# Optimization experiments

Hardware: AMD Instinct MI355X
Metric: run time of the kernel (lower is better)

The kernel has to match this reference:

```python
import jax, jax.numpy as jnp
import numpy as np

# ---- static ragged feature layout (from CTGAN metadata) ----
NUM_CLUSTERS = [10, 8, 10, 5, 10, 10, 7, 10, 10, 10]          # per numerical feature
NUM_CATEGORIES = [2, 5, 10, 3, 50, 4, 2, 8, 100, 6, 2, 3, 12, 5, 2, 30, 4, 9, 2, 7]
TAU = 0.2        # GumbelSoftmax temperature (teras default)
BN_EPS = 1e-3    # keras BatchNormalization default epsilon
LATENT_DIM = 128
BATCH = 65536

_seg, _alpha = [], []
_gid = 0
for c in NUM_CLUSTERS:
    _seg.append(_gid); _alpha.append(True); _gid += 1        # alpha scalar (tanh), own segment
    _seg += [_gid] * c; _alpha += [False] * c; _gid += 1     # beta cluster group (gumbel softmax)
for k in NUM_CATEGORIES:
    _seg += [_gid] * k; _alpha += [False] * k; _gid += 1     # categorical group (gumbel softmax)
SEG = jnp.asarray(np.array(_seg, dtype=np.int32))
ALPHA_MASK = jnp.asarray(np.array(_alpha, dtype=bool))
N_SEG = _gid
DATA_DIM = len(_seg)  # 366


def setup_inputs() -> dict:
    key = jax.random.key(0)
    ks = jax.random.split(key, 8)
    z = jax.random.normal(ks[0], (BATCH, LATENT_DIM), dtype=jnp.float32)
    # pre-sampled standard Gumbel noise for the gumbel-softmax groups
    u = jax.random.uniform(ks[1], (BATCH, DATA_DIM), dtype=jnp.float32, minval=1e-6, maxval=1.0 - 1e-6)
    g = -jnp.log(-jnp.log(u))
    def w(k, fi, fo):
        return jax.random.normal(k, (fi, fo), dtype=jnp.float32) * (1.0 / np.sqrt(fi))
    return {
        "z": z, "g": g,
        "W1": w(ks[2], LATENT_DIM, 256), "b1": jnp.zeros((256,), jnp.float32),
        "gamma1": jnp.ones((256,), jnp.float32), "beta1": jnp.zeros((256,), jnp.float32),
        "W2": w(ks[3], LATENT_DIM + 256, 256), "b2": jnp.zeros((256,), jnp.float32),
        "gamma2": jnp.ones((256,), jnp.float32), "beta2": jnp.zeros((256,), jnp.float32),
        "Wout": w(ks[4], LATENT_DIM + 512, DATA_DIM), "bout": jnp.zeros((DATA_DIM,), jnp.float32),
    }


def _bn_relu(h, gamma, beta):
    # training-mode batch norm (batch statistics), as used while training CTGAN
    mu = jnp.mean(h, axis=0)
    var = jnp.var(h, axis=0)
    return jax.nn.relu((h - mu) * jax.lax.rsqrt(var + BN_EPS) * gamma + beta)


def reference(z, g, W1, b1, gamma1, beta1, W2, b2, gamma2, beta2, Wout, bout):
    # CTGAN residual generator layers: out = concat([relu(bn(dense(x))), x])
    h1 = jnp.concatenate([_bn_relu(z @ W1 + b1, gamma1, beta1), z], axis=1)    # [B, 384]
    h2 = jnp.concatenate([_bn_relu(h1 @ W2 + b2, gamma2, beta2), h1], axis=1)  # [B, 640]
    logits = h2 @ Wout + bout                                                  # [B, 366]

    # ragged per-group gumbel-softmax: segment-wise stable softmax over columns
    zt = ((logits + g) / TAU).T                                   # [D, B]
    m = jax.ops.segment_max(zt, SEG, num_segments=N_SEG)          # [S, B]
    e = jnp.exp(zt - m[SEG])
    s = jax.ops.segment_sum(e, SEG, num_segments=N_SEG)
    soft = (e / s[SEG]).T                                         # [B, D]
    # alpha columns: tanh of raw logits; all other columns: group softmax
    return jnp.where(ALPHA_MASK[None, :], jnp.tanh(logits), soft)
```

## Files before the change

kernel.cpp:

```cpp
#include <hip/hip_runtime.h>

typedef _Float16 half_t;
typedef _Float16 half4 __attribute__((ext_vector_type(4)));
typedef _Float16 half8 __attribute__((ext_vector_type(8)));
typedef float f32x4 __attribute__((ext_vector_type(4)));

#define AS1 __attribute__((address_space(1)))
#define AS3 __attribute__((address_space(3)))

static constexpr int NBATCH = 65536;

__global__ __launch_bounds__(256) void k_cvtz(const float* __restrict__ z,
                                              half_t* __restrict__ dst) {
  size_t i = (size_t)blockIdx.x * 256 + threadIdx.x;
  int row = (int)(i >> 4), c8 = (int)(i & 15) << 3;
  const float* s = z + (size_t)row * 128 + c8;
  float4 v0 = *(const float4*)s;
  float4 v1 = *(const float4*)(s + 4);
  half8 h;
  h[0]=(half_t)v0.x; h[1]=(half_t)v0.y; h[2]=(half_t)v0.z; h[3]=(half_t)v0.w;
  h[4]=(half_t)v1.x; h[5]=(half_t)v1.y; h[6]=(half_t)v1.z; h[7]=(half_t)v1.w;
  *(half8*)(dst + (size_t)row * 640 + c8) = h;
}

__global__ __launch_bounds__(256) void k_transpose(const float* __restrict__ W,
                                                   half_t* __restrict__ Wt,
                                                   int K, int N, int total) {
  int i = blockIdx.x * 256 + threadIdx.x;
  if (i >= total) return;
  int n = i / K;
  int k = i - n * K;
  float v = (n < N) ? W[k * N + n] : 0.f;
  Wt[i] = (half_t)v;
}

template<bool STATS, bool F16OUT>
__global__ __launch_bounds__(256) void k_gemm(
    const half_t* __restrict__ A, int lda, int K,
    const half_t* __restrict__ Bt,
    const float* __restrict__ bias,
    half_t* __restrict__ o16, float* __restrict__ o32, int ldo, int ncreal,
    float* __restrict__ ps, float* __restrict__ pq) {
  __shared__ __align__(16) char smem[32768];
  const int tid  = threadIdx.x;
  const int lane = tid & 63;
  const int w    = tid >> 6;
  const int wr   = w >> 1, wc = w & 1;
  const int ml   = lane & 15, g = lane >> 4;
  const int brow = blockIdx.x * 128;
  const int bcol = blockIdx.y * 128;
  const int sr  = lane >> 3;
  const int scg = (lane & 7) ^ sr;

  f32x4 acc[4][4];
#pragma unroll
  for (int i = 0; i < 4; i++)
#pragma unroll
    for (int j = 0; j < 4; j++) acc[i][j] = (f32x4){0.f, 0.f, 0.f, 0.f};

  const half_t* Abase = A  + (size_t)brow * lda;
  const half_t* Bbase = Bt + (size_t)bcol * K;
  const int nt = K >> 6;

  half_t* As = (half_t*)smem;
  half_t* Bs = (half_t*)(smem + 16384);

  for (int t = 0; t < nt; t++) {
    const int k0 = t * 64;
    if (t) __syncthreads();
#pragma unroll
    for (int it = 0; it < 4; it++) {
      int q = it * 4 + w;
      int r = q * 8 + sr;
      __builtin_amdgcn_global_load_lds(
          (AS1 const void*)(Abase + (size_t)r * lda + k0 + scg * 8),
          (AS3 void*)(As + q * 512), 16, 0, 0);
      __builtin_amdgcn_global_load_lds(
          (AS1 const void*)(Bbase + (size_t)r * K + k0 + scg * 8),
          (AS3 void*)(Bs + q * 512), 16, 0, 0);
    }
    __syncthreads();
#pragma unroll
    for (int t2 = 0; t2 < 2; t2++) {
      const int c4 = t2 * 4 + g;
      half8 af[4], bf[4];
#pragma unroll
      for (int fm = 0; fm < 4; fm++) {
        int row = wr * 64 + fm * 16 + ml;
        af[fm] = *(const half8*)((const char*)As + row * 128 + ((c4 ^ (row & 7)) << 4));
      }
#pragma unroll
      for (int fn = 0; fn < 4; fn++) {
        int row = wc * 64 + fn * 16 + ml;
        bf[fn] = *(const half8*)((const char*)Bs + row * 128 + ((c4 ^ (row & 7)) << 4));
      }
#pragma unroll
      for (int fm = 0; fm < 4; fm++)
#pragma unroll
        for (int fn = 0; fn < 4; fn++)
          acc[fm][fn] = __builtin_amdgcn_mfma_f32_16x16x32_f16(af[fm], bf[fn], acc[fm][fn], 0, 0, 0);
    }
  }
  __syncthreads();

#pragma unroll
  for (int fn = 0; fn < 4; fn++) {
    int col  = wc * 64 + fn * 16 + ml;
    int gcol = bcol + col;
    float bz = (gcol < ncreal) ? bias[gcol] : 0.f;
    float s = 0.f, q = 0.f;
#pragma unroll
    for (int fm = 0; fm < 4; fm++)
#pragma unroll
      for (int rr = 0; rr < 4; rr++) {
        float v = acc[fm][fn][rr] + bz;
        acc[fm][fn][rr] = v;
        if (STATS) { s += v; q += v * v; }
      }
    if (STATS) {
      s += __shfl_xor(s, 16, 64); s += __shfl_xor(s, 32, 64);
      q += __shfl_xor(q, 16, 64); q += __shfl_xor(q, 32, 64);
      if (g == 0) {
        ps[(size_t)gcol * 1024 + blockIdx.x * 2 + wr] = s;
        pq[(size_t)gcol * 1024 + blockIdx.x * 2 + wr] = q;
      }
    }
  }

  if (F16OUT) {
    half_t* so = (half_t*)smem;
#pragma unroll
    for (int fn = 0; fn < 4; fn++)
#pragma unroll
      for (int fm = 0; fm < 4; fm++)
#pragma unroll
        for (int rr = 0; rr < 4; rr++)
          so[(wr * 64 + fm * 16 + g * 4 + rr) * 128 + wc * 64 + fn * 16 + ml] =
              (half_t)acc[fm][fn][rr];
    __syncthreads();
#pragma unroll
    for (int it = 0; it < 8; it++) {
      int r = it * 16 + (tid >> 4);
      int c = (tid & 15) * 8;
      *(half8*)(o16 + (size_t)(brow + r) * ldo + bcol + c) = *(const half8*)&so[r * 128 + c];
    }
  } else {
    float* so = (float*)smem;
    for (int h = 0; h < 2; h++) {
      if (wr == h) {
#pragma unroll
        for (int fn = 0; fn < 4; fn++)
#pragma unroll
          for (int fm = 0; fm < 4; fm++)
#pragma unroll
            for (int rr = 0; rr < 4; rr++)
              so[(fm * 16 + g * 4 + rr) * 128 + wc * 64 + fn * 16 + ml] = acc[fm][fn][rr];
      }
      __syncthreads();
      int r0 = h * 64;
      for (int i = tid; i < 64 * 64; i += 256) {
        int r  = i >> 6;
        int c2 = (i & 63) * 2;
        int gc = bcol + c2;
        if (gc < ncreal)
          *(float2*)(o32 + (size_t)(brow + r0 + r) * ldo + gc) = *(const float2*)&so[r * 128 + c2];
      }
      __syncthreads();
    }
  }
}

__global__ __launch_bounds__(256) void k_bnfinal(
    const float* __restrict__ ps, const float* __restrict__ pq,
    const float* __restrict__ gamma, const float* __restrict__ beta,
    float* __restrict__ sc, float* __restrict__ sh) {
  int c = blockIdx.x, t = threadIdx.x;
  float s = 0.f, q = 0.f;
#pragma unroll
  for (int i = 0; i < 4; i++) {
    s += ps[(size_t)c * 1024 + t + i * 256];
    q += pq[(size_t)c * 1024 + t + i * 256];
  }
#pragma unroll
  for (int o = 1; o < 64; o <<= 1) { s += __shfl_xor(s, o, 64); q += __shfl_xor(q, o, 64); }
  __shared__ float ss[4], qq[4];
  if ((t & 63) == 0) { ss[t >> 6] = s; qq[t >> 6] = q; }
  __syncthreads();
  if (t == 0) {
    s = ss[0] + ss[1] + ss[2] + ss[3];
    q = qq[0] + qq[1] + qq[2] + qq[3];
    float mu   = s * (1.f / NBATCH);
    float var  = fmaxf(q * (1.f / NBATCH) - mu * mu, 0.f);
    float rstd = rsqrtf(var + 1e-3f);
    float a = gamma[c] * rstd;
    sc[c] = a;
    sh[c] = beta[c] - mu * a;
  }
}

__global__ __launch_bounds__(256) void k_bnrelu(half_t* __restrict__ p,
                                                const float* __restrict__ sc,
                                                const float* __restrict__ sh) {
  size_t i = (size_t)blockIdx.x * 256 + threadIdx.x;
  int row = (int)(i >> 5), c8 = (int)(i & 31) << 3;
  half_t* a = p + (size_t)row * 640 + c8;
  half8 v = *(const half8*)a;
  half8 o;
#pragma unroll
  for (int j = 0; j < 8; j++)
    o[j] = (half_t)fmaxf(fmaf((float)v[j], sc[c8 + j], sh[c8 + j]), 0.f);
  *(half8*)a = o;
}

template<int L>
__device__ __forceinline__ void seg_rt(float* __restrict__ zr, int S) {
  float v[L];
#pragma unroll
  for (int j = 0; j < L; j++) v[j] = zr[S + j];
  float m0 = -1e30f, m1 = -1e30f, m2 = -1e30f, m3 = -1e30f;
#pragma unroll
  for (int j = 0; j < L; j++) {
    if ((j & 3) == 0) m0 = fmaxf(m0, v[j]);
    else if ((j & 3) == 1) m1 = fmaxf(m1, v[j]);
    else if ((j & 3) == 2) m2 = fmaxf(m2, v[j]);
    else m3 = fmaxf(m3, v[j]);
  }
  const float m = fmaxf(fmaxf(m0, m1), fmaxf(m2, m3));
  float s0 = 0.f, s1 = 0.f, s2 = 0.f, s3 = 0.f;
#pragma unroll
  for (int j = 0; j < L; j++) {
    float e = __expf(v[j] - m);
    v[j] = e;
    if ((j & 3) == 0) s0 += e;
    else if ((j & 3) == 1) s1 += e;
    else if ((j & 3) == 2) s2 += e;
    else s3 += e;
  }
  const float inv = 1.0f / ((s0 + s1) + (s2 + s3));
#pragma unroll
  for (int j = 0; j < L; j++) zr[S + j] = v[j] * inv;
}

template<int L>
__device__ __forceinline__ void seg_pad(float* __restrict__ zr, int S, int Lr) {
  float v[L];
#pragma unroll
  for (int j = 0; j < L; j++) v[j] = (j < Lr) ? zr[S + j] : -1e30f;
  float m = -1e30f;
#pragma unroll
  for (int j = 0; j < L; j++) m = fmaxf(m, v[j]);
  float s = 0.f;
#pragma unroll
  for (int j = 0; j < L; j++) {
    float e = __expf(v[j] - m);
    v[j] = e;
    s += e;
  }
  const float inv = 1.0f / s;
#pragma unroll
  for (int j = 0; j < L; j++)
    if (j < Lr) zr[S + j] = v[j] * inv;
}

template<int S, int L>
__device__ __forceinline__ void seg_split(float* __restrict__ zr, int par) {
  constexpr int H = L / 2;
  const int base = S + par * H;
  float v[H];
#pragma unroll
  for (int j = 0; j < H; j++) v[j] = zr[base + j];
  float m = -1e30f;
#pragma unroll
  for (int j = 0; j < H; j++) m = fmaxf(m, v[j]);
  m = fmaxf(m, __shfl_xor(m, 1, 64));
  float s = 0.f;
#pragma unroll
  for (int j = 0; j < H; j++) {
    float e = __expf(v[j] - m);
    v[j] = e;
    s += e;
  }
  s += __shfl_xor(s, 1, 64);
  const float inv = 1.0f / s;
#pragma unroll
  for (int j = 0; j < H; j++) zr[base + j] = v[j] * inv;
}

template<int H>
__device__ __forceinline__ void seg_quad(float* __restrict__ zr, int base, int n) {
  float v[H];
#pragma unroll
  for (int j = 0; j < H; j++) v[j] = (j < n) ? zr[base + j] : -1e30f;
  float m = -1e30f;
#pragma unroll
  for (int j = 0; j < H; j++) m = fmaxf(m, v[j]);
  m = fmaxf(m, __shfl_xor(m, 1, 64));
  m = fmaxf(m, __shfl_xor(m, 2, 64));
  float s = 0.f;
#pragma unroll
  for (int j = 0; j < H; j++) {
    float e = __expf(v[j] - m);
    v[j] = e;
    s += e;
  }
  s += __shfl_xor(s, 1, 64);
  s += __shfl_xor(s, 2, 64);
  const float inv = 1.0f / s;
#pragma unroll
  for (int j = 0; j < H; j++)
    if (j < n) zr[base + j] = v[j] * inv;
}

__device__ __forceinline__ bool is_alpha(int c) {
  const unsigned long long AM0 =
      (1ull << 0) | (1ull << 11) | (1ull << 20) | (1ull << 31) | (1ull << 37) |
      (1ull << 48) | (1ull << 59);
  const unsigned long long AM1 = (1ull << 3) | (1ull << 14) | (1ull << 25);
  if (c >= 90) return false;
  return (((c < 64) ? (AM0 >> c) : (AM1 >> (c - 64))) & 1ull) != 0ull;
}

__global__ __launch_bounds__(512, 2) void k_softmax(const float* __restrict__ g,
                                                    float* __restrict__ out) {
  __shared__ float zb[32][373];
  const int tid = threadIdx.x;
  const size_t gbase = (size_t)blockIdx.x * 32 * 366;
  for (int i2 = tid; i2 < 32 * 183; i2 += 512) {
    int e0 = i2 * 2;
    int r = e0 / 366;
    int c = e0 - r * 366;
    float2 lg = *(const float2*)(out + gbase + e0);
    float2 gg = *(const float2*)(g + gbase + e0);
    zb[r][c]     = is_alpha(c)     ? tanhf(lg.x) : (lg.x + gg.x) * 5.0f;
    zb[r][c + 1] = is_alpha(c + 1) ? tanhf(lg.y) : (lg.y + gg.y) * 5.0f;
  }
  __syncthreads();
  {
    const int lane = tid & 63;
    const int w    = tid >> 6;
    const int par  = lane & 1;
    if (w < 4) {
      const int quad = lane & 3;
      float* zr = &zb[(w & 1) * 16 + (lane >> 2)][0];
      if (w < 2) {
        seg_quad<25>(zr, 184 + quad * 25, 25);
      } else {
        seg_quad<13>(zr, 120 + quad * 13 - (quad >> 1) * (quad & 1), 13 - (quad >> 1));
        seg_rt<10>(zr, par ? 68 : 1);
      }
    } else {
      float* zr = &zb[lane >> 1][0];
      switch (w) {
        case 4: seg_split<314, 30>(zr, par);
                seg_rt<7>(zr, par ? 359 : 60);
                seg_rt<2>(zr, par ? 174 : 100);
                seg_rt<2>(zr, par ? 312 : 290); break;
        case 5: seg_rt<10>(zr, par ? 90 : 38);
                seg_rt<10>(zr, par ? 107 : 49);
                seg_pad<2>(zr, par ? 357 : 0, par ? 2 : 0); break;
        case 6: seg_pad<12>(zr, par ? 348 : 295, par ? 9 : 12);
                seg_pad<6>(zr, par ? 284 : 32, par ? 6 : 5);
                seg_rt<5>(zr, par ? 307 : 102); break;
        default: seg_rt<10>(zr, par ? 79 : 21);
                 seg_rt<8>(zr, par ? 176 : 12);
                 seg_rt<4>(zr, par ? 344 : 170);
                 seg_rt<3>(zr, par ? 292 : 117); break;
      }
    }
  }
  __syncthreads();
  for (int i2 = tid; i2 < 32 * 183; i2 += 512) {
    int e0 = i2 * 2;
    int r = e0 / 366;
    int c = e0 - r * 366;
    float2 o;
    o.x = zb[r][c];
    o.y = zb[r][c + 1];
    *(float2*)(out + gbase + e0) = o;
  }
}

extern "C" void kernel_launch(void* const* d_in, const int* in_sizes, int n_in,
                              void* d_out, int out_size, void* d_ws, size_t ws_size,
                              hipStream_t stream) {
  const float* z      = (const float*)d_in[0];
  const float* g      = (const float*)d_in[1];
  const float* W1     = (const float*)d_in[2];
  const float* b1     = (const float*)d_in[3];
  const float* gamma1 = (const float*)d_in[4];
  const float* beta1  = (const float*)d_in[5];
  const float* W2     = (const float*)d_in[6];
  const float* b2     = (const float*)d_in[7];
  const float* gamma2 = (const float*)d_in[8];
  const float* beta2  = (const float*)d_in[9];
  const float* Wout   = (const float*)d_in[10];
  const float* bout   = (const float*)d_in[11];
  float* out = (float*)d_out;
  char* ws = (char*)d_ws;

  size_t off = 0;
  half_t* act = (half_t*)(ws + off); off += (size_t)NBATCH * 640 * 2;
  half_t* W1t = (half_t*)(ws + off); off += (size_t)256 * 128 * 2;
  half_t* W2t = (half_t*)(ws + off); off += (size_t)256 * 384 * 2;
  half_t* Wot = (half_t*)(ws + off); off += (size_t)384 * 640 * 2;
  float*  ps  = (float*)(ws + off);  off += (size_t)256 * 1024 * 4;
  float*  pq  = (float*)(ws + off);  off += (size_t)256 * 1024 * 4;
  float*  sc1 = (float*)(ws + off);  off += 256 * 4;
  float*  sh1 = (float*)(ws + off);  off += 256 * 4;
  float*  sc2 = (float*)(ws + off);  off += 256 * 4;
  float*  sh2 = (float*)(ws + off);  off += 256 * 4;
  (void)ws_size; (void)in_sizes; (void)n_in; (void)out_size;

  k_cvtz<<<4096, 256, 0, stream>>>(z, act + 512);
  k_transpose<<<(256 * 128 + 255) / 256, 256, 0, stream>>>(W1, W1t, 128, 256, 256 * 128);
  k_transpose<<<(256 * 384 + 255) / 256, 256, 0, stream>>>(W2, W2t, 384, 256, 256 * 384);
  k_transpose<<<(384 * 640 + 255) / 256, 256, 0, stream>>>(Wout, Wot, 640, 366, 384 * 640);

  k_gemm<true, true><<<dim3(512, 2), 256, 0, stream>>>(
      act + 512, 640, 128, W1t, b1, act + 256, nullptr, 640, 256, ps, pq);
  k_bnfinal<<<256, 256, 0, stream>>>(ps, pq, gamma1, beta1, sc1, sh1);
  k_bnrelu<<<8192, 256, 0, stream>>>(act + 256, sc1, sh1);

  k_gemm<true, true><<<dim3(512, 2), 256, 0, stream>>>(
      act + 256, 640, 384, W2t, b2, act + 0, nullptr, 640, 256, ps, pq);
  k_bnfinal<<<256, 256, 0, stream>>>(ps, pq, gamma2, beta2, sc2, sh2);
  k_bnrelu<<<8192, 256, 0, stream>>>(act + 0, sc2, sh2);

  k_gemm<false, false><<<dim3(512, 3), 256, 0, stream>>>(
      act, 640, 640, Wot, bout, nullptr, out, 366, 366, nullptr, nullptr);

  k_softmax<<<NBATCH / 32, 512, 0, stream>>>(g, out);
}
```

Baseline: 199.4 us.

## Move tanh into GEMM epilogue and run segment softmax directly on global memory

The tanh for alpha columns moves into the output GEMM epilogue. The softmax kernel drops its shared-memory staging and instead reads logits and Gumbel noise straight from global memory per segment, writing results back in place. Occupancy hints rise from 2 to 6 blocks per SM. This removes the LDS round trip and two barriers. In exchange, global accesses become strided per-row, scalar and uncoalesced, which may hurt memory efficiency.

Measured after the change: 279.2 us. +40.0%, slower.

```diff
diff --git a/kernel.cpp b/kernel.cpp
--- a/kernel.cpp
+++ b/kernel.cpp
@@ -9,6 +9,15 @@
 #define AS3 __attribute__((address_space(3)))
 
 static constexpr int NBATCH = 65536;
+
+__device__ __forceinline__ bool is_alpha(int c) {
+  const unsigned long long AM0 =
+      (1ull << 0) | (1ull << 11) | (1ull << 20) | (1ull << 31) | (1ull << 37) |
+      (1ull << 48) | (1ull << 59);
+  const unsigned long long AM1 = (1ull << 3) | (1ull << 14) | (1ull << 25);
+  if (c >= 90) return false;
+  return (((c < 64) ? (AM0 >> c) : (AM1 >> (c - 64))) & 1ull) != 0ull;
+}
 
 __global__ __launch_bounds__(256) void k_cvtz(const float* __restrict__ z,
                                               half_t* __restrict__ dst) {
@@ -162,8 +171,14 @@
         int r  = i >> 6;
         int c2 = (i & 63) * 2;
         int gc = bcol + c2;
-        if (gc < ncreal)
-          *(float2*)(o32 + (size_t)(brow + r0 + r) * ldo + gc) = *(const float2*)&so[r * 128 + c2];
+        if (gc < ncreal) {
+          float2 v = *(const float2*)&so[r * 128 + c2];
+          if (gc < 90) {
+            if (is_alpha(gc))     v.x = tanhf(v.x);
+            if (is_alpha(gc + 1)) v.y = tanhf(v.y);
+          }
+          *(float2*)(o32 + (size_t)(brow + r0 + r) * ldo + gc) = v;
+        }
       }
       __syncthreads();
     }
@@ -213,84 +228,71 @@
 }
 
 template<int L>
-__device__ __forceinline__ void seg_rt(float* __restrict__ zr, int S) {
+__device__ __forceinline__ void gseg_rt(float* __restrict__ zo,
+                                        const float* __restrict__ zg, int S) {
   float v[L];
 #pragma unroll
-  for (int j = 0; j < L; j++) v[j] = zr[S + j];
-  float m0 = -1e30f, m1 = -1e30f, m2 = -1e30f, m3 = -1e30f;
-#pragma unroll
-  for (int j = 0; j < L; j++) {
-    if ((j & 3) == 0) m0 = fmaxf(m0, v[j]);
-    else if ((j & 3) == 1) m1 = fmaxf(m1, v[j]);
-    else if ((j & 3) == 2) m2 = fmaxf(m2, v[j]);
-    else m3 = fmaxf(m3, v[j]);
-  }
-  const float m = fmaxf(fmaxf(m0, m1), fmaxf(m2, m3));
-  float s0 = 0.f, s1 = 0.f, s2 = 0.f, s3 = 0.f;
-#pragma unroll
-  for (int j = 0; j < L; j++) {
-    float e = __expf(v[j] - m);
-    v[j] = e;
-    if ((j & 3) == 0) s0 += e;
-    else if ((j & 3) == 1) s1 += e;
-    else if ((j & 3) == 2) s2 += e;
-    else s3 += e;
-  }
-  const float inv = 1.0f / ((s0 + s1) + (s2 + s3));
-#pragma unroll
-  for (int j = 0; j < L; j++) zr[S + j] = v[j] * inv;
-}
-
-template<int L>
-__device__ __forceinline__ void seg_pad(float* __restrict__ zr, int S, int Lr) {
-  float v[L];
-#pragma unroll
-  for (int j = 0; j < L; j++) v[j] = (j < Lr) ? zr[S + j] : -1e30f;
+  for (int j = 0; j < L; j++) v[j] = (zo[S + j] + zg[S + j]) * 5.0f;
   float m = -1e30f;
 #pragma unroll
   for (int j = 0; j < L; j++) m = fmaxf(m, v[j]);
   float s = 0.f;
 #pragma unroll
-  for (int j = 0; j < L; j++) {
-    float e = __expf(v[j] - m);
-    v[j] = e;
-    s += e;
-  }
+  for (int j = 0; j < L; j++) { float e = __expf(v[j] - m); v[j] = e; s += e; }
   const float inv = 1.0f / s;
 #pragma unroll
+  for (int j = 0; j < L; j++) zo[S + j] = v[j] * inv;
+}
+
+template<int L>
+__device__ __forceinline__ void gseg_pad(float* __restrict__ zo,
+                                         const float* __restrict__ zg,
+                                         int S, int Lr) {
+  float v[L];
+#pragma unroll
   for (int j = 0; j < L; j++)
-    if (j < Lr) zr[S + j] = v[j] * inv;
+    v[j] = (j < Lr) ? (zo[S + j] + zg[S + j]) * 5.0f : -1e30f;
+  float m = -1e30f;
+#pragma unroll
+  for (int j = 0; j < L; j++) m = fmaxf(m, v[j]);
+  float s = 0.f;
+#pragma unroll
+  for (int j = 0; j < L; j++) { float e = __expf(v[j] - m); v[j] = e; s += e; }
+  const float inv = 1.0f / s;
+#pragma unroll
+  for (int j = 0; j < L; j++)
+    if (j < Lr) zo[S + j] = v[j] * inv;
 }
 
 template<int S, int L>
-__device__ __forceinline__ void seg_split(float* __restrict__ zr, int par) {
+__device__ __forceinline__ void gseg_split(float* __restrict__ zo,
+                                           const float* __restrict__ zg, int par) {
   constexpr int H = L / 2;
-  const int base = S + par * H;
+  const int b = S + par * H;
   float v[H];
 #pragma unroll
-  for (int j = 0; j < H; j++) v[j] = zr[base + j];
+  for (int j = 0; j < H; j++) v[j] = (zo[b + j] + zg[b + j]) * 5.0f;
   float m = -1e30f;
 #pragma unroll
   for (int j = 0; j < H; j++) m = fmaxf(m, v[j]);
   m = fmaxf(m, __shfl_xor(m, 1, 64));
   float s = 0.f;
 #pragma unroll
-  for (int j = 0; j < H; j++) {
-    float e = __expf(v[j] - m);
-    v[j] = e;
-    s += e;
-  }
+  for (int j = 0; j < H; j++) { float e = __expf(v[j] - m); v[j] = e; s += e; }
   s += __shfl_xor(s, 1, 64);
   const float inv = 1.0f / s;
 #pragma unroll
-  for (int j = 0; j < H; j++) zr[base + j] = v[j] * inv;
+  for (int j = 0; j < H; j++) zo[b + j] = v[j] * inv;
 }
 
 template<int H>
-__device__ __forceinline__ void seg_quad(float* __restrict__ zr, int base, int n) {
+__device__ __forceinline__ void gseg_quad(float* __restrict__ zo,
+                                          const float* __restrict__ zg,
+                                          int b, int n) {
   float v[H];
 #pragma unroll
-  for (int j = 0; j < H; j++) v[j] = (j < n) ? zr[base + j] : -1e30f;
+  for (int j = 0; j < H; j++)
+    v[j] = (j < n) ? (zo[b + j] + zg[b + j]) * 5.0f : -1e30f;
   float m = -1e30f;
 #pragma unroll
   for (int j = 0; j < H; j++) m = fmaxf(m, v[j]);
@@ -298,85 +300,54 @@
   m = fmaxf(m, __shfl_xor(m, 2, 64));
   float s = 0.f;
 #pragma unroll
-  for (int j = 0; j < H; j++) {
-    float e = __expf(v[j] - m);
-    v[j] = e;
-    s += e;
-  }
+  for (int j = 0; j < H; j++) { float e = __expf(v[j] - m); v[j] = e; s += e; }
   s += __shfl_xor(s, 1, 64);
   s += __shfl_xor(s, 2, 64);
   const float inv = 1.0f / s;
 #pragma unroll
   for (int j = 0; j < H; j++)
-    if (j < n) zr[base + j] = v[j] * inv;
-}
-
-__device__ __forceinline__ bool is_alpha(int c) {
-  const unsigned long long AM0 =
-      (1ull << 0) | (1ull << 11) | (1ull << 20) | (1ull << 31) | (1ull << 37) |
-      (1ull << 48) | (1ull << 59);
-  const unsigned long long AM1 = (1ull << 3) | (1ull << 14) | (1ull << 25);
-  if (c >= 90) return false;
-  return (((c < 64) ? (AM0 >> c) : (AM1 >> (c - 64))) & 1ull) != 0ull;
-}
-
-__global__ __launch_bounds__(512, 2) void k_softmax(const float* __restrict__ g,
+    if (j < n) zo[b + j] = v[j] * inv;
+}
+
+__global__ __launch_bounds__(512, 6) void k_softmax(const float* __restrict__ g,
                                                     float* __restrict__ out) {
-  __shared__ float zb[32][373];
-  const int tid = threadIdx.x;
+  const int tid  = threadIdx.x;
+  const int lane = tid & 63;
+  const int w    = tid >> 6;
   const size_t gbase = (size_t)blockIdx.x * 32 * 366;
-  for (int i2 = tid; i2 < 32 * 183; i2 += 512) {
-    int e0 = i2 * 2;
-    int r = e0 / 366;
-    int c = e0 - r * 366;
-    float2 lg = *(const float2*)(out + gbase + e0);
-    float2 gg = *(const float2*)(g + gbase + e0);
-    zb[r][c]     = is_alpha(c)     ? tanhf(lg.x) : (lg.x + gg.x) * 5.0f;
-    zb[r][c + 1] = is_alpha(c + 1) ? tanhf(lg.y) : (lg.y + gg.y) * 5.0f;
-  }
-  __syncthreads();
-  {
-    const int lane = tid & 63;
-    const int w    = tid >> 6;
-    const int par  = lane & 1;
-    if (w < 4) {
-      const int quad = lane & 3;
-      float* zr = &zb[(w & 1) * 16 + (lane >> 2)][0];
-      if (w < 2) {
-        seg_quad<25>(zr, 184 + quad * 25, 25);
-      } else {
-        seg_quad<13>(zr, 120 + quad * 13 - (quad >> 1) * (quad & 1), 13 - (quad >> 1));
-        seg_rt<10>(zr, par ? 68 : 1);
-      }
+  if (w < 4) {
+    const int quad = lane & 3;
+    const int row  = (w & 1) * 16 + (lane >> 2);
+    float* zo = out + gbase + (size_t)row * 366;
+    const float* zg = g + gbase + (size_t)row * 366;
+    if (w < 2) {
+      gseg_quad<25>(zo, zg, 184 + quad * 25, 25);
     } else {
-      float* zr = &zb[lane >> 1][0];
-      switch (w) {
-        case 4: seg_split<314, 30>(zr, par);
-                seg_rt<7>(zr, par ? 359 : 60);
-                seg_rt<2>(zr, par ? 174 : 100);
-                seg_rt<2>(zr, par ? 312 : 290); break;
-        case 5: seg_rt<10>(zr, par ? 90 : 38);
-                seg_rt<10>(zr, par ? 107 : 49);
-                seg_pad<2>(zr, par ? 357 : 0, par ? 2 : 0); break;
-        case 6: seg_pad<12>(zr, par ? 348 : 295, par ? 9 : 12);
-                seg_pad<6>(zr, par ? 284 : 32, par ? 6 : 5);
-                seg_rt<5>(zr, par ? 307 : 102); break;
-        default: seg_rt<10>(zr, par ? 79 : 21);
-                 seg_rt<8>(zr, par ? 176 : 12);
-                 seg_rt<4>(zr, par ? 344 : 170);
-                 seg_rt<3>(zr, par ? 292 : 117); break;
-      }
-    }
-  }
-  __syncthreads();
-  for (int i2 = tid; i2 < 32 * 183; i2 += 512) {
-    int e0 = i2 * 2;
-    int r = e0 / 366;
-    int c = e0 - r * 366;
-    float2 o;
-    o.x = zb[r][c];
-    o.y = zb[r][c + 1];
-    *(float2*)(out + gbase + e0) = o;
+      gseg_quad<13>(zo, zg, 120 + quad * 13 - (quad >> 1) * (quad & 1),
+                    13 - (quad >> 1));
+      gseg_rt<10>(zo, zg, (lane & 1) ? 68 : 1);
+    }
+  } else {
+    const int par = lane & 1;
+    const int row = lane >> 1;
+    float* zo = out + gbase + (size_t)row * 366;
+    const float* zg = g + gbase + (size_t)row * 366;
+    switch (w) {
+      case 4: gseg_split<314, 30>(zo, zg, par);
+              gseg_rt<7>(zo, zg, par ? 359 : 60);
+              gseg_rt<2>(zo, zg, par ? 174 : 100);
+              gseg_rt<2>(zo, zg, par ? 312 : 290); break;
+      case 5: gseg_rt<10>(zo, zg, par ? 90 : 38);
+              gseg_rt<10>(zo, zg, par ? 107 : 49);
+              gseg_pad<2>(zo, zg, par ? 357 : 0, par ? 2 : 0); break;
+      case 6: gseg_pad<12>(zo, zg, par ? 348 : 295, par ? 9 : 12);
+              gseg_pad<6>(zo, zg, par ? 284 : 32, par ? 6 : 5);
+              gseg_rt<5>(zo, zg, par ? 307 : 102); break;
+      default: gseg_rt<10>(zo, zg, par ? 79 : 21);
+               gseg_rt<8>(zo, zg, par ? 176 : 12);
+               gseg_rt<4>(zo, zg, par ? 344 : 170);
+               gseg_rt<3>(zo, zg, par ? 292 : 117); break;
+    }
   }
 }
 
```
